# Optimization experiments

Measured on AMD Instinct MI355X. Metric: run time of the kernel, lower is better.

Reference implementation:

```python
import jax, jax.numpy as jnp
import numpy as np

N = 100000   # nodes
E = 1600000  # edges
D = 128      # feature dim
G = 64       # graphs in batch


def setup_inputs() -> dict:
    key = jax.random.key(0)
    k1, k2, k3, k4, k5, k6, k7, k8 = jax.random.split(key, 8)
    in_feat = jax.random.normal(k1, (N, D), dtype=jnp.float32)
    src = jax.random.randint(k2, (E,), 0, N, dtype=jnp.int32)
    dst = jax.random.randint(k3, (E,), 0, N, dtype=jnp.int32)
    graph_ids = jax.random.randint(k4, (N,), 0, G, dtype=jnp.int32)
    s = 1.0 / np.sqrt(D)
    W1 = jax.random.uniform(k5, (D, D), jnp.float32, -s, s)
    b1 = jnp.zeros((D,), jnp.float32)
    W2 = jax.random.uniform(k6, (D, D), jnp.float32, -s, s)
    b2 = jnp.zeros((D,), jnp.float32)
    return {"in_feat": in_feat, "W1": W1, "b1": b1, "W2": W2, "b2": b2,
            "src": src, "dst": dst, "graph_ids": graph_ids}


def _graph_conv(x, src, dst, W, b, norm_src, norm_dst):
    # DGL GraphConv, norm='both': D_out^{-1/2} A D_in^{-1/2} X W + b
    m = (x * norm_src[:, None])[src]                       # [E, d] gather
    agg = jax.ops.segment_sum(m, dst, num_segments=N)      # [N, d] scatter-add
    return (agg * norm_dst[:, None]) @ W + b


def reference(in_feat, W1, b1, W2, b2, src, dst, graph_ids):
    ones_e = jnp.ones((E,), jnp.float32)
    deg_out = jax.ops.segment_sum(ones_e, src, num_segments=N)
    deg_in = jax.ops.segment_sum(ones_e, dst, num_segments=N)
    norm_src = jnp.where(deg_out > 0, deg_out, 1.0) ** -0.5  # D_out^{-1/2}
    norm_dst = jnp.where(deg_in > 0, deg_in, 1.0) ** -0.5    # D_in^{-1/2}

    h = _graph_conv(in_feat, src, dst, W1, b1, norm_src, norm_dst)
    h = jax.nn.relu(h)
    h = _graph_conv(h, src, dst, W2, b2, norm_src, norm_dst)

    # AvgPooling: per-graph mean over nodes -> [G, D]
    sums = jax.ops.segment_sum(h, graph_ids, num_segments=G)
    counts = jax.ops.segment_sum(jnp.ones((N,), jnp.float32), graph_ids, num_segments=G)
    return sums / jnp.maximum(counts, 1.0)[:, None]
```

## Files before the change

### kernel.cpp

```cpp
#include <hip/hip_runtime.h>
#include <cstdint>


#define DD 128
#define PB 512
#define GB 384
#define KC 32
#define CHK 3200

typedef __attribute__((ext_vector_type(8))) short bf16x8;
typedef __attribute__((ext_vector_type(4))) float f32x4;
typedef __attribute__((ext_vector_type(2))) float f32x2;

__device__ __forceinline__ unsigned short f2bf(float f) {
  union { float f; unsigned u; } v; v.f = f;
  unsigned r = (v.u + 0x7fff + ((v.u >> 16) & 1)) >> 16;
  return (unsigned short)r;
}
__device__ __forceinline__ unsigned char f2fp8(float f) {
  return (unsigned char)(__builtin_amdgcn_cvt_pk_fp8_f32(f, f, 0, false) & 0xff);
}

__global__ __launch_bounds__(256) void k_part1a(const int* __restrict__ src, const int* __restrict__ dst,
                                                const int* __restrict__ gid,
                                                unsigned* __restrict__ histD, unsigned* __restrict__ histS,
                                                unsigned* __restrict__ rawD, unsigned* __restrict__ rawS,
                                                int* __restrict__ gcnt, int E, int N, int G) {
  __shared__ unsigned hD[256], hS[256];
  __shared__ int h64[64];
  hD[threadIdx.x] = 0; hS[threadIdx.x] = 0;
  if (threadIdx.x < 64) h64[threadIdx.x] = 0;
  __syncthreads();
  int chunk = (E + gridDim.x - 1) / gridDim.x;
  int e0 = blockIdx.x * chunk, e1 = min(E, e0 + chunk);
  for (int e = e0 + threadIdx.x; e < e1; e += 256) {
    atomicAdd(&hD[(unsigned)dst[e] >> 9], 1u);
    atomicAdd(&hS[(unsigned)src[e] >> 9], 1u);
  }
  int stride = gridDim.x * 256;
  for (int i = blockIdx.x * 256 + threadIdx.x; i < N; i += stride)
    atomicAdd(&h64[gid[i]], 1);
  __syncthreads();
  unsigned vd = hD[threadIdx.x], vs = hS[threadIdx.x];
  histD[blockIdx.x * 256 + threadIdx.x] = vd;
  histS[blockIdx.x * 256 + threadIdx.x] = vs;
  rawD[blockIdx.x * 256 + threadIdx.x] = vd;
  rawS[blockIdx.x * 256 + threadIdx.x] = vs;
  if (threadIdx.x < (unsigned)G) {
    int v = h64[threadIdx.x];
    if (v) atomicAdd(&gcnt[threadIdx.x], v);
  }
}

__global__ __launch_bounds__(256) void k_pscanA(unsigned* __restrict__ histD, unsigned* __restrict__ histS,
                                                unsigned* __restrict__ tot) {
  __shared__ unsigned excl[PB], psc[256];
  int table = blockIdx.x >> 8, b = blockIdx.x & 255;
  unsigned* hist = table ? histS : histD;
  int t = threadIdx.x;
  unsigned s0 = hist[(2 * t) * 256 + b];
  unsigned s1 = hist[(2 * t + 1) * 256 + b];
  unsigned pr = s0 + s1;
  psc[t] = pr;
  __syncthreads();
  for (int off = 1; off < 256; off <<= 1) {
    unsigned x = (t >= off) ? psc[t - off] : 0;
    __syncthreads();
    psc[t] += x;
    __syncthreads();
  }
  unsigned pex = psc[t] - pr;
  excl[2 * t] = pex;
  excl[2 * t + 1] = pex + s0;
  __syncthreads();
  hist[(2 * t) * 256 + b] = excl[2 * t];
  hist[(2 * t + 1) * 256 + b] = excl[2 * t + 1];
  if (t == 255) tot[table * 256 + b] = psc[255];
}

__global__ __launch_bounds__(256) void k_pscanB(const unsigned* __restrict__ tot,
                                                int* __restrict__ bsD, int* __restrict__ bsS) {
  __shared__ unsigned s[256];
  int t = threadIdx.x;
#pragma unroll
  for (int table = 0; table < 2; ++table) {
    int* bs = table ? bsS : bsD;
    unsigned v = tot[table * 256 + t];
    s[t] = v;
    __syncthreads();
    for (int off = 1; off < 256; off <<= 1) {
      unsigned x = (t >= off) ? s[t - off] : 0;
      __syncthreads();
      s[t] += x;
      __syncthreads();
    }
    bs[t] = (int)(s[t] - v);
    if (t == 255) bs[256] = (int)s[255];
    __syncthreads();
  }
}

__global__ __launch_bounds__(256) void k_pscanC(unsigned* __restrict__ histD, unsigned* __restrict__ histS,
                                                const int* __restrict__ bsD, const int* __restrict__ bsS) {
  int table = blockIdx.x >> 9, i = blockIdx.x & (PB - 1);
  unsigned* hist = table ? histS : histD;
  const int* bs = table ? bsS : bsD;
  hist[i * 256 + threadIdx.x] += (unsigned)bs[threadIdx.x];
}

__global__ __launch_bounds__(256) void k_part1c(const int* __restrict__ src, const int* __restrict__ dst,
                                                const unsigned* __restrict__ histD, const unsigned* __restrict__ histS,
                                                const unsigned* __restrict__ rawD, const unsigned* __restrict__ rawS,
                                                unsigned* __restrict__ pairD, unsigned* __restrict__ pairS, int E) {
  __shared__ unsigned pkD[CHK], pkS[CHK];
  __shared__ unsigned char bkD[CHK], bkS[CHK];
  __shared__ unsigned curD[256], curS[256], gbD[256], gbS[256], psc[256];
  int chunk = (E + gridDim.x - 1) / gridDim.x;
  int e0 = blockIdx.x * chunk, e1 = min(E, e0 + chunk);
  int n = e1 - e0;
  int t = threadIdx.x;
  unsigned vD = rawD[blockIdx.x * 256 + t];
  psc[t] = vD;
  __syncthreads();
  for (int off = 1; off < 256; off <<= 1) {
    unsigned x = (t >= off) ? psc[t - off] : 0;
    __syncthreads();
    psc[t] += x;
    __syncthreads();
  }
  unsigned exD = psc[t] - vD;
  curD[t] = exD;
  gbD[t] = histD[blockIdx.x * 256 + t] - exD;
  __syncthreads();
  unsigned vS = rawS[blockIdx.x * 256 + t];
  psc[t] = vS;
  __syncthreads();
  for (int off = 1; off < 256; off <<= 1) {
    unsigned x = (t >= off) ? psc[t - off] : 0;
    __syncthreads();
    psc[t] += x;
    __syncthreads();
  }
  unsigned exS = psc[t] - vS;
  curS[t] = exS;
  gbS[t] = histS[blockIdx.x * 256 + t] - exS;
  __syncthreads();
  for (int i = t; i < n; i += 256) {
    unsigned sv = (unsigned)src[e0 + i], dv = (unsigned)dst[e0 + i];
    unsigned bD = dv >> 9, bS = sv >> 9;
    unsigned pD = atomicAdd(&curD[bD], 1u);
    pkD[pD] = ((dv & 511u) << 17) | sv;
    bkD[pD] = (unsigned char)bD;
    unsigned pS = atomicAdd(&curS[bS], 1u);
    pkS[pS] = ((sv & 511u) << 17) | dv;
    bkS[pS] = (unsigned char)bS;
  }
  __syncthreads();
  for (int i = t; i < n; i += 256)
    pairD[gbD[bkD[i]] + i] = pkD[i];
  for (int i = t; i < n; i += 256)
    pairS[gbS[bkS[i]] + i] = pkS[i];
}

__global__ __launch_bounds__(256) void k_part2d(const unsigned* __restrict__ pairD, const int* __restrict__ bsD,
                                                const int* __restrict__ gcnt, const int* __restrict__ gid,
                                                int* __restrict__ offs, float* __restrict__ ndst,
                                                uint2* __restrict__ pwg,
                                                int* __restrict__ srcS, int N) {
  __shared__ unsigned hist[512], excl[512], psc[256];
  int k = blockIdx.x, base = k << 9;
  int b0 = bsD[k], b1 = bsD[k + 1];
  hist[threadIdx.x] = 0; hist[threadIdx.x + 256] = 0;
  __syncthreads();
  for (int i = b0 + threadIdx.x; i < b1; i += 256)
    atomicAdd(&hist[pairD[i] >> 17], 1u);
  __syncthreads();
  unsigned s0 = hist[2 * threadIdx.x], s1 = hist[2 * threadIdx.x + 1];
  unsigned pr = s0 + s1;
  psc[threadIdx.x] = pr;
  __syncthreads();
  for (int off = 1; off < 256; off <<= 1) {
    unsigned x = (threadIdx.x >= off) ? psc[threadIdx.x - off] : 0;
    __syncthreads();
    psc[threadIdx.x] += x;
    __syncthreads();
  }
  unsigned pex = psc[threadIdx.x] - pr;
  excl[2 * threadIdx.x] = pex;
  excl[2 * threadIdx.x + 1] = pex + s0;
  __syncthreads();
  for (int j = threadIdx.x; j < 512; j += 256) {
    int node = base + j;
    if (node <= N) offs[node] = b0 + (int)excl[j];
    if (node < N) {
      float gi = (float)hist[j]; gi = gi > 0.f ? gi : 1.f;
      float nd = rsqrtf(gi);
      ndst[node] = nd;
      float c = (float)gcnt[gid[node]]; c = c > 1.f ? c : 1.f;
      float w = nd / c;
      union { float f; unsigned u; } v; v.f = w;
      pwg[node] = make_uint2(v.u, (unsigned)gid[node]);
    }
  }
  __syncthreads();
  for (int i = b0 + threadIdx.x; i < b1; i += 256) {
    unsigned pkv = pairD[i];
    unsigned pos = atomicAdd(&excl[pkv >> 17], 1u);
    srcS[b0 + (int)pos] = (int)(pkv & 0x1FFFFu);
  }
}

__global__ __launch_bounds__(1024, 1) void k_pw(const unsigned* __restrict__ pairS, const int* __restrict__ bsS,
                                                const uint2* __restrict__ pwg,
                                                unsigned short* __restrict__ P16,
                                                float* __restrict__ nsrc, int N) {
  __shared__ float tile[512 * 64];
  __shared__ unsigned hist[512];
  int k = blockIdx.x, base = k << 9;
  int b0 = bsS[k], b1 = bsS[k + 1];
  for (int i = threadIdx.x; i < 512 * 64; i += 1024) tile[i] = 0.f;
  if (threadIdx.x < 512) hist[threadIdx.x] = 0;
  __syncthreads();
  for (int i = b0 + threadIdx.x; i < b1; i += 1024) {
    unsigned pkv = pairS[i];
    unsigned dv = pkv & 0x1FFFFu;
    unsigned sloc = pkv >> 17;
    atomicAdd(&hist[sloc], 1u);
    uint2 u = pwg[dv];
    union { unsigned u; float f; } w; w.u = u.x;
    atomicAdd(&tile[sloc * 64 + u.y], w.f);
  }
  __syncthreads();
  if (threadIdx.x < 512) {
    int node = base + threadIdx.x;
    if (node < N) {
      float g = (float)hist[threadIdx.x]; g = g > 0.f ? g : 1.f;
      nsrc[node] = rsqrtf(g);
    }
  }
  for (int grp = threadIdx.x; grp < 4096; grp += 1024) {
    int qb = grp >> 6, g = grp & 63;
    unsigned w0 = (unsigned)f2bf(tile[(qb * 8 + 0) * 64 + g]) | ((unsigned)f2bf(tile[(qb * 8 + 1) * 64 + g]) << 16);
    unsigned w1 = (unsigned)f2bf(tile[(qb * 8 + 2) * 64 + g]) | ((unsigned)f2bf(tile[(qb * 8 + 3) * 64 + g]) << 16);
    unsigned w2 = (unsigned)f2bf(tile[(qb * 8 + 4) * 64 + g]) | ((unsigned)f2bf(tile[(qb * 8 + 5) * 64 + g]) << 16);
    unsigned w3 = (unsigned)f2bf(tile[(qb * 8 + 6) * 64 + g]) | ((unsigned)f2bf(tile[(qb * 8 + 7) * 64 + g]) << 16);
    uint4 o = make_uint4(w0, w1, w2, w3);
    *(uint4*)(P16 + ((size_t)(base >> 3) + qb) * 512 + g * 8) = o;
  }
}

__global__ __launch_bounds__(128) void k_wprep(const float* __restrict__ W, unsigned short* __restrict__ Wt) {
  int n = blockIdx.x, k = threadIdx.x;
  Wt[n * 128 + k] = f2bf(W[k * 128 + n]);
}

__global__ __launch_bounds__(256) void k_gemm1(const float* __restrict__ X, const unsigned short* __restrict__ Wt,
                                               const float* __restrict__ nsrc,
                                               unsigned char* __restrict__ Z8, int N) {
  int wave = threadIdx.x >> 6, lane = threadIdx.x & 63;
  int quad = lane >> 4, l16 = lane & 15;
  int row0 = blockIdx.x * 64 + wave * 16;
  int arow = row0 + l16; if (arow >= N) arow = N - 1;
  const float* xr = X + (size_t)arow * 128 + quad * 8;
  f32x4 acc[8];
#pragma unroll
  for (int i = 0; i < 8; ++i) acc[i] = (f32x4){0.f, 0.f, 0.f, 0.f};
#pragma unroll
  for (int kb = 0; kb < 128; kb += 32) {
    float4 x0 = *(const float4*)(xr + kb);
    float4 x1 = *(const float4*)(xr + kb + 4);
    bf16x8 a;
    a[0] = (short)f2bf(x0.x); a[1] = (short)f2bf(x0.y);
    a[2] = (short)f2bf(x0.z); a[3] = (short)f2bf(x0.w);
    a[4] = (short)f2bf(x1.x); a[5] = (short)f2bf(x1.y);
    a[6] = (short)f2bf(x1.z); a[7] = (short)f2bf(x1.w);
#pragma unroll
    for (int nt = 0; nt < 8; ++nt) {
      bf16x8 b = *(const bf16x8*)(Wt + (size_t)(nt * 16 + l16) * 128 + kb + quad * 8);
      acc[nt] = __builtin_amdgcn_mfma_f32_16x16x32_bf16(a, b, acc[nt], 0, 0, 0);
    }
  }
  int rbase = row0 + quad * 4;
#pragma unroll
  for (int r = 0; r < 4; ++r) {
    int row = rbase + r;
    if (row < N) {
      float s = nsrc[row];
#pragma unroll
      for (int nt = 0; nt < 8; ++nt)
        Z8[(size_t)row * 128 + nt * 16 + l16] = f2fp8(acc[nt][r] * s);
    }
  }
}

#define ACCP(u) do {                                              \
    c0 += __builtin_amdgcn_cvt_pk_f32_fp8((u).x, false);          \
    c1 += __builtin_amdgcn_cvt_pk_f32_fp8((u).x, true);           \
    c2 += __builtin_amdgcn_cvt_pk_f32_fp8((u).y, false);          \
    c3 += __builtin_amdgcn_cvt_pk_f32_fp8((u).y, true);           \
  } while (0)

__global__ __launch_bounds__(256) void k_layer1(const unsigned char* __restrict__ Z8,
                                                const int* __restrict__ offs, const int* __restrict__ srcS,
                                                const float* __restrict__ b1,
                                                const float* __restrict__ nsrc, const float* __restrict__ ndst,
                                                unsigned short* __restrict__ Hb, int N) {
  int lane = threadIdx.x & 63;
  int q = lane >> 4, l16 = lane & 15;
  int d = blockIdx.x * 16 + (threadIdx.x >> 6) * 4 + q;
  bool live = d < N;
  int dc = live ? d : N - 1;
  int start = offs[dc];
  int end = live ? offs[dc + 1] : start;
  const int boff = l16 * 8;
  const unsigned char* zb = Z8 + boff;
  float4 bv0 = *(const float4*)(b1 + boff);
  float4 bv1 = *(const float4*)(b1 + boff + 4);
  float nd = ndst[dc], ns = nsrc[dc];
  f32x2 c0 = {0.f, 0.f}, c1 = {0.f, 0.f}, c2 = {0.f, 0.f}, c3 = {0.f, 0.f};
  int e = start;
  int rem = end - start;
  int s0 = 0, s1 = 0, s2 = 0, s3 = 0;
  if (rem > 0) s0 = srcS[e];
  if (rem > 1) s1 = srcS[e + 1];
  if (rem > 2) s2 = srcS[e + 2];
  if (rem > 3) s3 = srcS[e + 3];
  while (__any(rem > 0)) {
    uint2 u0 = make_uint2(0u, 0u), u1 = make_uint2(0u, 0u);
    uint2 u2 = make_uint2(0u, 0u), u3 = make_uint2(0u, 0u);
    if (rem > 0) u0 = *(const uint2*)(zb + ((size_t)s0 << 7));
    if (rem > 1) u1 = *(const uint2*)(zb + ((size_t)s1 << 7));
    if (rem > 2) u2 = *(const uint2*)(zb + ((size_t)s2 << 7));
    if (rem > 3) u3 = *(const uint2*)(zb + ((size_t)s3 << 7));
    if (rem > 4) s0 = srcS[e + 4];
    if (rem > 5) s1 = srcS[e + 5];
    if (rem > 6) s2 = srcS[e + 6];
    if (rem > 7) s3 = srcS[e + 7];
    ACCP(u0);
    ACCP(u1);
    ACCP(u2);
    ACCP(u3);
    e += 4;
    rem -= 4;
  }
  if (live) {
    float h0 = fmaxf(fmaf(nd, c0[0], bv0.x), 0.f) * ns;
    float h1 = fmaxf(fmaf(nd, c0[1], bv0.y), 0.f) * ns;
    float h2 = fmaxf(fmaf(nd, c1[0], bv0.z), 0.f) * ns;
    float h3 = fmaxf(fmaf(nd, c1[1], bv0.w), 0.f) * ns;
    float h4 = fmaxf(fmaf(nd, c2[0], bv1.x), 0.f) * ns;
    float h5 = fmaxf(fmaf(nd, c2[1], bv1.y), 0.f) * ns;
    float h6 = fmaxf(fmaf(nd, c3[0], bv1.z), 0.f) * ns;
    float h7 = fmaxf(fmaf(nd, c3[1], bv1.w), 0.f) * ns;
    unsigned w0 = (unsigned)f2bf(h0) | ((unsigned)f2bf(h1) << 16);
    unsigned w1 = (unsigned)f2bf(h2) | ((unsigned)f2bf(h3) << 16);
    unsigned w2 = (unsigned)f2bf(h4) | ((unsigned)f2bf(h5) << 16);
    unsigned w3 = (unsigned)f2bf(h6) | ((unsigned)f2bf(h7) << 16);
    *(uint4*)(Hb + (size_t)d * 128 + boff) = make_uint4(w0, w1, w2, w3);
  }
}

__global__ __launch_bounds__(256) void k_poolgemm(const unsigned short* __restrict__ P16,
                                                  const unsigned short* __restrict__ Hb,
                                                  float* __restrict__ pooled, int N, int Kpad, int chunk) {
  __shared__ unsigned short Hl[KC * 128];
  int t = threadIdx.x;
  int r0 = blockIdx.x * chunk;
  int r1 = min(Kpad, r0 + chunk);
  int wv = t >> 6, lane = t & 63, quad = lane >> 4, l16 = lane & 15;
  f32x4 acc[8];
#pragma unroll
  for (int i = 0; i < 8; ++i) acc[i] = (f32x4){0.f, 0.f, 0.f, 0.f};
  for (int rb = r0; rb < r1; rb += KC) {
    int r = t >> 3, c = (t & 7) * 16;
    int cs = c ^ ((r >> 3) * 16);
    int row = rb + r;
    if (row < N) {
      const uint4* srcp = (const uint4*)(Hb + (size_t)row * 128 + c);
      *(uint4*)(Hl + r * 128 + cs) = srcp[0];
      *(uint4*)(Hl + r * 128 + cs + 8) = srcp[1];
    } else {
      uint4 z = make_uint4(0, 0, 0, 0);
      *(uint4*)(Hl + r * 128 + cs) = z;
      *(uint4*)(Hl + r * 128 + cs + 8) = z;
    }
    __syncthreads();
    bf16x8 a = *(const bf16x8*)(P16 + ((size_t)(rb >> 3) + quad) * 512 + (wv * 16 + l16) * 8);
#pragma unroll
    for (int ft = 0; ft < 8; ++ft) {
      bf16x8 b;
#pragma unroll
      for (int j = 0; j < 8; ++j) {
        int rr = quad * 8 + j;
        b[j] = (short)Hl[rr * 128 + ((ft ^ (rr >> 3)) * 16) + l16];
      }
      acc[ft] = __builtin_amdgcn_mfma_f32_16x16x32_bf16(a, b, acc[ft], 0, 0, 0);
    }
    __syncthreads();
  }
#pragma unroll
  for (int ft = 0; ft < 8; ++ft)
#pragma unroll
    for (int rg = 0; rg < 4; ++rg)
      unsafeAtomicAdd(&pooled[(wv * 16 + quad * 4 + rg) * DD + ft * 16 + l16], acc[ft][rg]);
}

__global__ __launch_bounds__(128) void k_out(const float* __restrict__ pooled, const float* __restrict__ W2,
                                             const float* __restrict__ b2, float* __restrict__ out) {
  __shared__ float p[DD];
  int g = blockIdx.x, d = threadIdx.x;
  p[d] = pooled[g * DD + d];
  __syncthreads();
  float a = b2[d];
#pragma unroll 4
  for (int k = 0; k < DD; ++k) a = fmaf(p[k], W2[k * DD + d], a);
  out[g * DD + d] = a;
}

extern "C" void kernel_launch(void* const* d_in, const int* in_sizes, int n_in,
                              void* d_out, int out_size, void* d_ws, size_t ws_size,
                              hipStream_t stream) {
  const float* X  = (const float*)d_in[0];
  const float* W1 = (const float*)d_in[1];
  const float* b1 = (const float*)d_in[2];
  const float* W2 = (const float*)d_in[3];
  const float* b2 = (const float*)d_in[4];
  const int* src  = (const int*)d_in[5];
  const int* dst  = (const int*)d_in[6];
  const int* gid  = (const int*)d_in[7];
  int E = in_sizes[5];
  int N = in_sizes[7];
  int G = out_size / DD;
  int nb = (N >> 9) + 1;
  int Kpad = nb << 9;
  int chunk = ((Kpad + GB * KC - 1) / (GB * KC)) * KC;

  char* w = (char*)d_ws;
  size_t o = 0;
  auto carve = [&](size_t bytes) { char* p = w + o; o += (bytes + 255) & ~(size_t)255; return p; };
  int*   gcnt   = (int*)  carve((size_t)G * 4);
  float* pooled = (float*)carve((size_t)G * DD * 4);
  size_t zeroBytes = o;
  unsigned* histD = (unsigned*)carve((size_t)PB * 256 * 4);
  unsigned* histS = (unsigned*)carve((size_t)PB * 256 * 4);
  unsigned* rawD  = (unsigned*)carve((size_t)PB * 256 * 4);
  unsigned* rawS  = (unsigned*)carve((size_t)PB * 256 * 4);
  unsigned* tot   = (unsigned*)carve(512 * 4);
  int*   bsD    = (int*)  carve(257 * 4);
  int*   bsS    = (int*)  carve(257 * 4);
  unsigned* pairD = (unsigned*)carve((size_t)E * 4);
  unsigned* pairS = (unsigned*)carve((size_t)E * 4);
  int*   srcS   = (int*)  carve((size_t)E * 4);
  int*   offs   = (int*)  carve((size_t)(N + 1) * 4);
  float* nsrc   = (float*)carve((size_t)N * 4);
  float* ndst   = (float*)carve((size_t)N * 4);
  uint2* pwg    = (uint2*)carve((size_t)N * 8);
  unsigned short* Wt = (unsigned short*)carve(128 * 128 * 2);
  unsigned char*  Z8 = (unsigned char*)carve((size_t)N * DD);
  unsigned short* Hb = (unsigned short*)carve((size_t)N * DD * 2);
  unsigned short* P16 = (unsigned short*)carve((size_t)Kpad * 64 * 2);

  hipMemsetAsync(d_ws, 0, zeroBytes, stream);

  k_part1a<<<PB, 256, 0, stream>>>(src, dst, gid, histD, histS, rawD, rawS, gcnt, E, N, G);
  k_pscanA<<<512, 256, 0, stream>>>(histD, histS, tot);
  k_pscanB<<<1, 256, 0, stream>>>(tot, bsD, bsS);
  k_pscanC<<<2 * PB, 256, 0, stream>>>(histD, histS, bsD, bsS);
  k_part1c<<<PB, 256, 0, stream>>>(src, dst, histD, histS, rawD, rawS, pairD, pairS, E);
  k_part2d<<<nb, 256, 0, stream>>>(pairD, bsD, gcnt, gid, offs, ndst, pwg, srcS, N);
  k_pw<<<nb, 1024, 0, stream>>>(pairS, bsS, pwg, P16, nsrc, N);
  k_wprep<<<128, 128, 0, stream>>>(W1, Wt);
  k_gemm1<<<(N + 63) / 64, 256, 0, stream>>>(X, Wt, nsrc, Z8, N);
  k_layer1<<<(N + 15) / 16, 256, 0, stream>>>(Z8, offs, srcS, b1, nsrc, ndst, Hb, N);
  k_poolgemm<<<GB, 256, 0, stream>>>(P16, Hb, pooled, N, Kpad, chunk);
  k_out<<<G, DD, 0, stream>>>(pooled, W2, b2, (float*)d_out);
}
```

Baseline: 291.8 us.

## Sort layer-1 destinations by in-degree and use packed bf16 conversion

Adds a degree-bucketed permutation of destination nodes, built from a histogram, a scan and a scatter, so that each wave in the layer-1 gather processes nodes of similar in-degree and lanes idle less. A zero padding row is appended to Z8 so the gather loop can load without per-edge predicates. Software bf16 rounding is replaced with the hardware v_cvt_pk_bf16_f32 instruction. The cost is two extra small kernel launches, extra atomics, and Hb rows written in scattered order.

```diff
diff --git a/kernel.cpp b/kernel.cpp
--- a/kernel.cpp
+++ b/kernel.cpp
@@ -16,6 +16,11 @@
   union { float f; unsigned u; } v; v.f = f;
   unsigned r = (v.u + 0x7fff + ((v.u >> 16) & 1)) >> 16;
   return (unsigned short)r;
+}
+__device__ __forceinline__ unsigned cvt_pk_bf16(float lo, float hi) {
+  unsigned r;
+  asm("v_cvt_pk_bf16_f32 %0, %1, %2" : "=v"(r) : "v"(lo), "v"(hi));
+  return r;
 }
 __device__ __forceinline__ unsigned char f2fp8(float f) {
   return (unsigned char)(__builtin_amdgcn_cvt_pk_fp8_f32(f, f, 0, false) & 0xff);
@@ -165,12 +170,15 @@
 __global__ __launch_bounds__(256) void k_part2d(const unsigned* __restrict__ pairD, const int* __restrict__ bsD,
                                                 const int* __restrict__ gcnt, const int* __restrict__ gid,
                                                 int* __restrict__ offs, float* __restrict__ ndst,
-                                                uint2* __restrict__ pwg,
+                                                uint2* __restrict__ pwg, int* __restrict__ degI,
+                                                int* __restrict__ dbin,
                                                 int* __restrict__ srcS, int N) {
   __shared__ unsigned hist[512], excl[512], psc[256];
+  __shared__ int ldb[256];
   int k = blockIdx.x, base = k << 9;
   int b0 = bsD[k], b1 = bsD[k + 1];
   hist[threadIdx.x] = 0; hist[threadIdx.x + 256] = 0;
+  ldb[threadIdx.x] = 0;
   __syncthreads();
   for (int i = b0 + threadIdx.x; i < b1; i += 256)
     atomicAdd(&hist[pairD[i] >> 17], 1u);
@@ -193,7 +201,10 @@
     int node = base + j;
     if (node <= N) offs[node] = b0 + (int)excl[j];
     if (node < N) {
-      float gi = (float)hist[j]; gi = gi > 0.f ? gi : 1.f;
+      int dg = (int)hist[j];
+      degI[node] = dg;
+      atomicAdd(&ldb[255 - min(dg, 255)], 1);
+      float gi = (float)dg; gi = gi > 0.f ? gi : 1.f;
       float nd = rsqrtf(gi);
       ndst[node] = nd;
       float c = (float)gcnt[gid[node]]; c = c > 1.f ? c : 1.f;
@@ -203,10 +214,47 @@
     }
   }
   __syncthreads();
+  if (ldb[threadIdx.x]) atomicAdd(&dbin[threadIdx.x], ldb[threadIdx.x]);
   for (int i = b0 + threadIdx.x; i < b1; i += 256) {
     unsigned pkv = pairD[i];
     unsigned pos = atomicAdd(&excl[pkv >> 17], 1u);
     srcS[b0 + (int)pos] = (int)(pkv & 0x1FFFFu);
+  }
+}
+
+__global__ __launch_bounds__(256) void k_dscan(const int* __restrict__ dbin, int* __restrict__ dcur) {
+  __shared__ int s[256];
+  int t = threadIdx.x;
+  int v = dbin[t];
+  s[t] = v;
+  __syncthreads();
+  for (int off = 1; off < 256; off <<= 1) {
+    int x = (t >= off) ? s[t - off] : 0;
+    __syncthreads();
+    s[t] += x;
+    __syncthreads();
+  }
+  dcur[t] = s[t] - v;
+}
+
+__global__ __launch_bounds__(256) void k_dperm(const int* __restrict__ degI, int* __restrict__ dcur,
+                                               int* __restrict__ perm, int N) {
+  __shared__ int lh[256], lcur[256];
+  int t = threadIdx.x, i = blockIdx.x * 256 + t;
+  lh[t] = 0;
+  __syncthreads();
+  int bin = 0;
+  if (i < N) {
+    bin = 255 - min(degI[i], 255);
+    atomicAdd(&lh[bin], 1);
+  }
+  __syncthreads();
+  int r = lh[t] ? atomicAdd(&dcur[t], lh[t]) : 0;
+  lcur[t] = r;
+  __syncthreads();
+  if (i < N) {
+    int pos = atomicAdd(&lcur[bin], 1);
+    perm[pos] = i;
   }
 }
 
@@ -240,18 +288,20 @@
   }
   for (int grp = threadIdx.x; grp < 4096; grp += 1024) {
     int qb = grp >> 6, g = grp & 63;
-    unsigned w0 = (unsigned)f2bf(tile[(qb * 8 + 0) * 64 + g]) | ((unsigned)f2bf(tile[(qb * 8 + 1) * 64 + g]) << 16);
-    unsigned w1 = (unsigned)f2bf(tile[(qb * 8 + 2) * 64 + g]) | ((unsigned)f2bf(tile[(qb * 8 + 3) * 64 + g]) << 16);
-    unsigned w2 = (unsigned)f2bf(tile[(qb * 8 + 4) * 64 + g]) | ((unsigned)f2bf(tile[(qb * 8 + 5) * 64 + g]) << 16);
-    unsigned w3 = (unsigned)f2bf(tile[(qb * 8 + 6) * 64 + g]) | ((unsigned)f2bf(tile[(qb * 8 + 7) * 64 + g]) << 16);
+    unsigned w0 = cvt_pk_bf16(tile[(qb * 8 + 0) * 64 + g], tile[(qb * 8 + 1) * 64 + g]);
+    unsigned w1 = cvt_pk_bf16(tile[(qb * 8 + 2) * 64 + g], tile[(qb * 8 + 3) * 64 + g]);
+    unsigned w2 = cvt_pk_bf16(tile[(qb * 8 + 4) * 64 + g], tile[(qb * 8 + 5) * 64 + g]);
+    unsigned w3 = cvt_pk_bf16(tile[(qb * 8 + 6) * 64 + g], tile[(qb * 8 + 7) * 64 + g]);
     uint4 o = make_uint4(w0, w1, w2, w3);
     *(uint4*)(P16 + ((size_t)(base >> 3) + qb) * 512 + g * 8) = o;
   }
 }
 
-__global__ __launch_bounds__(128) void k_wprep(const float* __restrict__ W, unsigned short* __restrict__ Wt) {
+__global__ __launch_bounds__(128) void k_wprep(const float* __restrict__ W, unsigned short* __restrict__ Wt,
+                                               unsigned char* __restrict__ zrow) {
   int n = blockIdx.x, k = threadIdx.x;
   Wt[n * 128 + k] = f2bf(W[k * 128 + n]);
+  if (n == 0) zrow[k] = 0;
 }
 
 __global__ __launch_bounds__(256) void k_gemm1(const float* __restrict__ X, const unsigned short* __restrict__ Wt,
@@ -269,15 +319,15 @@
   for (int kb = 0; kb < 128; kb += 32) {
     float4 x0 = *(const float4*)(xr + kb);
     float4 x1 = *(const float4*)(xr + kb + 4);
-    bf16x8 a;
-    a[0] = (short)f2bf(x0.x); a[1] = (short)f2bf(x0.y);
-    a[2] = (short)f2bf(x0.z); a[3] = (short)f2bf(x0.w);
-    a[4] = (short)f2bf(x1.x); a[5] = (short)f2bf(x1.y);
-    a[6] = (short)f2bf(x1.z); a[7] = (short)f2bf(x1.w);
+    union { unsigned u[4]; bf16x8 v; } A;
+    A.u[0] = cvt_pk_bf16(x0.x, x0.y);
+    A.u[1] = cvt_pk_bf16(x0.z, x0.w);
+    A.u[2] = cvt_pk_bf16(x1.x, x1.y);
+    A.u[3] = cvt_pk_bf16(x1.z, x1.w);
 #pragma unroll
     for (int nt = 0; nt < 8; ++nt) {
       bf16x8 b = *(const bf16x8*)(Wt + (size_t)(nt * 16 + l16) * 128 + kb + quad * 8);
-      acc[nt] = __builtin_amdgcn_mfma_f32_16x16x32_bf16(a, b, acc[nt], 0, 0, 0);
+      acc[nt] = __builtin_amdgcn_mfma_f32_16x16x32_bf16(A.v, b, acc[nt], 0, 0, 0);
     }
   }
   int rbase = row0 + quad * 4;
@@ -302,44 +352,45 @@
 
 __global__ __launch_bounds__(256) void k_layer1(const unsigned char* __restrict__ Z8,
                                                 const int* __restrict__ offs, const int* __restrict__ srcS,
+                                                const int* __restrict__ perm,
                                                 const float* __restrict__ b1,
                                                 const float* __restrict__ nsrc, const float* __restrict__ ndst,
                                                 unsigned short* __restrict__ Hb, int N) {
   int lane = threadIdx.x & 63;
   int q = lane >> 4, l16 = lane & 15;
-  int d = blockIdx.x * 16 + (threadIdx.x >> 6) * 4 + q;
-  bool live = d < N;
-  int dc = live ? d : N - 1;
-  int start = offs[dc];
-  int end = live ? offs[dc + 1] : start;
+  int dd = blockIdx.x * 16 + (threadIdx.x >> 6) * 4 + q;
+  bool live = dd < N;
+  int pd = perm[live ? dd : 0];
+  int start = offs[pd];
+  int end = live ? offs[pd + 1] : start;
   const int boff = l16 * 8;
   const unsigned char* zb = Z8 + boff;
   float4 bv0 = *(const float4*)(b1 + boff);
   float4 bv1 = *(const float4*)(b1 + boff + 4);
-  float nd = ndst[dc], ns = nsrc[dc];
+  float nd = ndst[pd], ns = nsrc[pd];
   f32x2 c0 = {0.f, 0.f}, c1 = {0.f, 0.f}, c2 = {0.f, 0.f}, c3 = {0.f, 0.f};
   int e = start;
   int rem = end - start;
-  int s0 = 0, s1 = 0, s2 = 0, s3 = 0;
+  int s0 = N, s1 = N, s2 = N, s3 = N;
   if (rem > 0) s0 = srcS[e];
   if (rem > 1) s1 = srcS[e + 1];
   if (rem > 2) s2 = srcS[e + 2];
   if (rem > 3) s3 = srcS[e + 3];
   while (__any(rem > 0)) {
-    uint2 u0 = make_uint2(0u, 0u), u1 = make_uint2(0u, 0u);
-    uint2 u2 = make_uint2(0u, 0u), u3 = make_uint2(0u, 0u);
-    if (rem > 0) u0 = *(const uint2*)(zb + ((size_t)s0 << 7));
-    if (rem > 1) u1 = *(const uint2*)(zb + ((size_t)s1 << 7));
-    if (rem > 2) u2 = *(const uint2*)(zb + ((size_t)s2 << 7));
-    if (rem > 3) u3 = *(const uint2*)(zb + ((size_t)s3 << 7));
-    if (rem > 4) s0 = srcS[e + 4];
-    if (rem > 5) s1 = srcS[e + 5];
-    if (rem > 6) s2 = srcS[e + 6];
-    if (rem > 7) s3 = srcS[e + 7];
+    uint2 u0 = *(const uint2*)(zb + ((size_t)s0 << 7));
+    uint2 u1 = *(const uint2*)(zb + ((size_t)s1 << 7));
+    uint2 u2 = *(const uint2*)(zb + ((size_t)s2 << 7));
+    uint2 u3 = *(const uint2*)(zb + ((size_t)s3 << 7));
+    int n0 = N, n1 = N, n2 = N, n3 = N;
+    if (rem > 4) n0 = srcS[e + 4];
+    if (rem > 5) n1 = srcS[e + 5];
+    if (rem > 6) n2 = srcS[e + 6];
+    if (rem > 7) n3 = srcS[e + 7];
     ACCP(u0);
     ACCP(u1);
     ACCP(u2);
     ACCP(u3);
+    s0 = n0; s1 = n1; s2 = n2; s3 = n3;
     e += 4;
     rem -= 4;
   }
@@ -352,11 +403,11 @@
     float h5 = fmaxf(fmaf(nd, c2[1], bv1.y), 0.f) * ns;
     float h6 = fmaxf(fmaf(nd, c3[0], bv1.z), 0.f) * ns;
     float h7 = fmaxf(fmaf(nd, c3[1], bv1.w), 0.f) * ns;
-    unsigned w0 = (unsigned)f2bf(h0) | ((unsigned)f2bf(h1) << 16);
-    unsigned w1 = (unsigned)f2bf(h2) | ((unsigned)f2bf(h3) << 16);
-    unsigned w2 = (unsigned)f2bf(h4) | ((unsigned)f2bf(h5) << 16);
-    unsigned w3 = (unsigned)f2bf(h6) | ((unsigned)f2bf(h7) << 16);
-    *(uint4*)(Hb + (size_t)d * 128 + boff) = make_uint4(w0, w1, w2, w3);
+    unsigned w0 = cvt_pk_bf16(h0, h1);
+    unsigned w1 = cvt_pk_bf16(h2, h3);
+    unsigned w2 = cvt_pk_bf16(h4, h5);
+    unsigned w3 = cvt_pk_bf16(h6, h7);
+    *(uint4*)(Hb + (size_t)pd * 128 + boff) = make_uint4(w0, w1, w2, w3);
   }
 }
 
@@ -440,6 +491,7 @@
   auto carve = [&](size_t bytes) { char* p = w + o; o += (bytes + 255) & ~(size_t)255; return p; };
   int*   gcnt   = (int*)  carve((size_t)G * 4);
   float* pooled = (float*)carve((size_t)G * DD * 4);
+  int*   dbin   = (int*)  carve(256 * 4);
   size_t zeroBytes = o;
   unsigned* histD = (unsigned*)carve((size_t)PB * 256 * 4);
   unsigned* histS = (unsigned*)carve((size_t)PB * 256 * 4);
@@ -448,15 +500,18 @@
   unsigned* tot   = (unsigned*)carve(512 * 4);
   int*   bsD    = (int*)  carve(257 * 4);
   int*   bsS    = (int*)  carve(257 * 4);
+  int*   dcur   = (int*)  carve(256 * 4);
   unsigned* pairD = (unsigned*)carve((size_t)E * 4);
   unsigned* pairS = (unsigned*)carve((size_t)E * 4);
   int*   srcS   = (int*)  carve((size_t)E * 4);
   int*   offs   = (int*)  carve((size_t)(N + 1) * 4);
+  int*   degI   = (int*)  carve((size_t)N * 4);
+  int*   perm   = (int*)  carve((size_t)N * 4);
   float* nsrc   = (float*)carve((size_t)N * 4);
   float* ndst   = (float*)carve((size_t)N * 4);
   uint2* pwg    = (uint2*)carve((size_t)N * 8);
   unsigned short* Wt = (unsigned short*)carve(128 * 128 * 2);
-  unsigned char*  Z8 = (unsigned char*)carve((size_t)N * DD);
+  unsigned char*  Z8 = (unsigned char*)carve((size_t)(N + 1) * DD);
   unsigned short* Hb = (unsigned short*)carve((size_t)N * DD * 2);
   unsigned short* P16 = (unsigned short*)carve((size_t)Kpad * 64 * 2);
 
@@ -467,11 +522,13 @@
   k_pscanB<<<1, 256, 0, stream>>>(tot, bsD, bsS);
   k_pscanC<<<2 * PB, 256, 0, stream>>>(histD, histS, bsD, bsS);
   k_part1c<<<PB, 256, 0, stream>>>(src, dst, histD, histS, rawD, rawS, pairD, pairS, E);
-  k_part2d<<<nb, 256, 0, stream>>>(pairD, bsD, gcnt, gid, offs, ndst, pwg, srcS, N);
+  k_part2d<<<nb, 256, 0, stream>>>(pairD, bsD, gcnt, gid, offs, ndst, pwg, degI, dbin, srcS, N);
+  k_dscan<<<1, 256, 0, stream>>>(dbin, dcur);
+  k_dperm<<<(N + 255) / 256, 256, 0, stream>>>(degI, dcur, perm, N);
   k_pw<<<nb, 1024, 0, stream>>>(pairS, bsS, pwg, P16, nsrc, N);
-  k_wprep<<<128, 128, 0, stream>>>(W1, Wt);
+  k_wprep<<<128, 128, 0, stream>>>(W1, Wt, Z8 + (size_t)N * DD);
   k_gemm1<<<(N + 63) / 64, 256, 0, stream>>>(X, Wt, nsrc, Z8, N);
-  k_layer1<<<(N + 15) / 16, 256, 0, stream>>>(Z8, offs, srcS, b1, nsrc, ndst, Hb, N);
+  k_layer1<<<(N + 15) / 16, 256, 0, stream>>>(Z8, offs, srcS, perm, b1, nsrc, ndst, Hb, N);
   k_poolgemm<<<GB, 256, 0, stream>>>(P16, Hb, pooled, N, Kpad, chunk);
   k_out<<<G, DD, 0, stream>>>(pooled, W2, b2, (float*)d_out);
 }
```

Result: no change. 293.1 us (+0.4%).
